# Kernel tuning notes

Hardware: AMD Instinct MI355X
Metric: run time of the kernel (lower is better)

The kernel has to match this reference:

```python
import jax, jax.numpy as jnp
import numpy as np

T = 100          # sequence length (number of GRU steps)
H = 50           # carry/hidden dim
Z = 10           # latent dim
OUT = Z + Z * (Z + 1) // 2  # 65: mean + tril Cholesky entries
LN_EPS = 1e-6    # flax LayerNorm default epsilon


def setup_inputs() -> dict:
    key = jax.random.key(0)
    ks = jax.random.split(key, 8)
    # Orthogonal-ish recurrent kernels via QR for well-conditioned dynamics
    def ortho(k):
        a = jax.random.normal(k, (H, H), dtype=jnp.float32)
        q, _ = jnp.linalg.qr(a)
        return q
    return {
        "carry_init": jax.random.normal(ks[0], (H,), dtype=jnp.float32),
        "W_hr": ortho(ks[1]), "b_hr": jnp.zeros((H,), jnp.float32),
        "s_r": jnp.ones((H,), jnp.float32), "o_r": jnp.zeros((H,), jnp.float32),
        "W_hz": ortho(ks[2]), "b_hz": jnp.zeros((H,), jnp.float32),
        "s_z": jnp.ones((H,), jnp.float32), "o_z": jnp.zeros((H,), jnp.float32),
        "W_hn": ortho(ks[3]), "b_hn": jnp.zeros((H,), jnp.float32),
        "s_n": jnp.ones((H,), jnp.float32), "o_n": jnp.zeros((H,), jnp.float32),
        "W_dense": jax.random.normal(ks[4], (H, OUT), jnp.float32) * (1.0 / jnp.sqrt(H)),
        "b_dense": jnp.zeros((OUT,), jnp.float32),
    }


def _layernorm(x, scale, bias):
    mu = jnp.mean(x, axis=-1, keepdims=True)
    var = jnp.mean(jnp.square(x - mu), axis=-1, keepdims=True)
    return (x - mu) * jax.lax.rsqrt(var + LN_EPS) * scale + bias


def reference(carry_init, W_hr, b_hr, s_r, o_r, W_hz, b_hz, s_z, o_z,
              W_hn, b_hn, s_n, o_n, W_dense, b_dense):
    # Input to the GRU is zeros((T,1)) -> cell ignores it entirely (no input kernel).
    def step(h, _):
        r = jax.nn.sigmoid(_layernorm(h @ W_hr + b_hr, s_r, o_r))
        z = jax.nn.sigmoid(_layernorm(h @ W_hz + b_hz, s_z, o_z))
        n = jnp.tanh(r * _layernorm(h @ W_hn + b_hn, s_n, o_n))
        new_h = (1.0 - z) * n + z * h
        return new_h, new_h

    _, hs = jax.lax.scan(step, carry_init, None, length=T)  # (T, H)
    out = hs @ W_dense + b_dense                              # (T, OUT)

    tril = jnp.tril_indices(Z)
    eye = jnp.eye(Z, dtype=out.dtype)

    def nat(x):
        mu, flat = x[:Z], x[Z:]
        L = jnp.zeros((Z, Z), dtype=x.dtype).at[tril].set(flat)
        d = jax.nn.softplus(jnp.diagonal(L))  # positive diagonal -> PD Sigma
        L = L.at[jnp.diag_indices(Z)].set(d)
        Sigma = L @ L.T
        # psd_solve: J = Sigma^{-1} via Cholesky solve
        J = jax.scipy.linalg.cho_solve((L, True), eye)
        h_nat = J @ mu
        return Sigma, mu, J, h_nat

    Sigma, mu, J, h_nat = jax.vmap(nat)(out)
    return Sigma, mu, J, h_nat
```

## Files before the change

### kernel.cpp

```cpp
#include <hip/hip_runtime.h>
#include <hip/hip_bf16.h>
#include <math.h>

#define T_STEPS 100
#define H_DIM   50
#define Z_DIM   10
#define OUT_DIM 65
#define KP      25

typedef _Float16 half2v __attribute__((ext_vector_type(2)));

__device__ __forceinline__ float bcast_lane(float v, int lane) {
    return __uint_as_float(__builtin_amdgcn_readlane(__float_as_uint(v), lane));
}
__device__ __forceinline__ unsigned readlane_u(unsigned v, int lane) {
    return (unsigned)__builtin_amdgcn_readlane((int)v, lane);
}
template<int CTRL>
__device__ __forceinline__ float dpp_mov(float x) {
    return __uint_as_float((unsigned)__builtin_amdgcn_update_dpp(
        0, (int)__float_as_uint(x), CTRL, 0xF, 0xF, true));
}
#define DPP_ROW_SHL1 0x101
#define DPP_SHR1     0x111
#define DPP_SHR2     0x112
#define DPP_SHR4     0x114
#define DPP_SHR8     0x118
#define DPP_BCAST15  0x142
#define DPP_BCAST31  0x143

__device__ __forceinline__ unsigned pack_h2(float lo, float hi) {
#if __has_builtin(__builtin_amdgcn_cvt_pkrtz)
    return __builtin_bit_cast(unsigned, __builtin_amdgcn_cvt_pkrtz(lo, hi));
#else
    half2v p; p.x = (_Float16)lo; p.y = (_Float16)hi;
    return __builtin_bit_cast(unsigned, p);
#endif
}
__device__ __forceinline__ float fdot2h(unsigned a, unsigned b, float c) {
#if __has_builtin(__builtin_amdgcn_fdot2)
    return __builtin_amdgcn_fdot2(__builtin_bit_cast(half2v, a),
                                  __builtin_bit_cast(half2v, b), c, false);
#else
    const half2v x = __builtin_bit_cast(half2v, a);
    const half2v y = __builtin_bit_cast(half2v, b);
    return fmaf((float)x.x, (float)y.x, fmaf((float)x.y, (float)y.y, c));
#endif
}

__device__ __forceinline__ float fast_rcp(float x) { return __builtin_amdgcn_rcpf(x); }
__device__ __forceinline__ float fast_rsq(float x) { return __builtin_amdgcn_rsqf(x); }
__device__ __forceinline__ float fast_sigmoid(float x) {
    return fast_rcp(1.0f + __expf(-x));
}
__device__ __forceinline__ float fast_tanh(float y) {
    return 1.0f - 2.0f * fast_rcp(__expf(2.0f * y) + 1.0f);
}

__global__ __launch_bounds__(64, 1)
void gru_recur_kernel(
    const float* __restrict__ carry_init,
    const float* __restrict__ W_hr, const float* __restrict__ b_hr,
    const float* __restrict__ s_r,  const float* __restrict__ o_r,
    const float* __restrict__ W_hz, const float* __restrict__ b_hz,
    const float* __restrict__ s_z,  const float* __restrict__ o_z,
    const float* __restrict__ W_hn, const float* __restrict__ b_hn,
    const float* __restrict__ s_n,  const float* __restrict__ o_n,
    float* __restrict__ ws_h)
{
    const int  j     = threadIdx.x;
    const bool valid = (j < H_DIM);
    const int  jc    = valid ? j : 0;

    unsigned wr[KP], wz[KP], wn[KP];
    #pragma unroll
    for (int k = 0; k < KP; ++k) {
        const int i0 = 2 * k, i1 = 2 * k + 1;
        wr[k] = pack_h2(valid ? W_hr[i0 * H_DIM + j] : 0.0f,
                        valid ? W_hr[i1 * H_DIM + j] : 0.0f);
        wz[k] = pack_h2(valid ? W_hz[i0 * H_DIM + j] : 0.0f,
                        valid ? W_hz[i1 * H_DIM + j] : 0.0f);
        wn[k] = pack_h2(valid ? W_hn[i0 * H_DIM + j] : 0.0f,
                        valid ? W_hn[i1 * H_DIM + j] : 0.0f);
    }
    #pragma unroll
    for (int k = 0; k < KP; ++k)
        asm volatile("" : "+v"(wr[k]), "+v"(wz[k]), "+v"(wn[k]));

    const float bjr = valid ? b_hr[jc] : 0.0f;
    const float bjz = valid ? b_hz[jc] : 0.0f;
    const float bjn = valid ? b_hn[jc] : 0.0f;
    const float sr  = s_r[jc], og_r = o_r[jc];
    const float sz  = s_z[jc], og_z = o_z[jc];
    const float sn  = s_n[jc], og_n = o_n[jc];

    float h = valid ? carry_init[jc] : 0.0f;
    const float invH = 1.0f / (float)H_DIM;

    float    hsl = dpp_mov<DPP_ROW_SHL1>(h);
    unsigned hpk = pack_h2(h, hsl);

    #pragma unroll 1
    for (int t = 0; t < T_STEPS; ++t) {
        float ar0 = bjr, ar1 = 0.0f;
        float az0 = bjz, az1 = 0.0f;
        float an0 = bjn, an1 = 0.0f;
        #pragma unroll
        for (int k = 0; k < KP; k += 2) {
            const unsigned s0 = readlane_u(hpk, 2 * k);
            ar0 = fdot2h(s0, wr[k], ar0);
            az0 = fdot2h(s0, wz[k], az0);
            an0 = fdot2h(s0, wn[k], an0);
            if (k + 1 < KP) {
                const unsigned s1 = readlane_u(hpk, 2 * (k + 1));
                ar1 = fdot2h(s1, wr[k + 1], ar1);
                az1 = fdot2h(s1, wz[k + 1], az1);
                an1 = fdot2h(s1, wn[k + 1], an1);
            }
        }
        const float ar = ar0 + ar1;
        const float az = az0 + az1;
        const float an = an0 + an1;

        float mr = ar, qr = ar * ar;
        float mz = az, qz = az * az;
        float mn = an, qn = an * an;
        #define STAGE(C)                                      \
            mr += dpp_mov<C>(mr); qr += dpp_mov<C>(qr);       \
            mz += dpp_mov<C>(mz); qz += dpp_mov<C>(qz);       \
            mn += dpp_mov<C>(mn); qn += dpp_mov<C>(qn);
        STAGE(DPP_SHR1) STAGE(DPP_SHR2) STAGE(DPP_SHR4)
        STAGE(DPP_SHR8) STAGE(DPP_BCAST15) STAGE(DPP_BCAST31)
        #undef STAGE
        mr = bcast_lane(mr, 63); qr = bcast_lane(qr, 63);
        mz = bcast_lane(mz, 63); qz = bcast_lane(qz, 63);
        mn = bcast_lane(mn, 63); qn = bcast_lane(qn, 63);

        const float mu_r  = mr * invH;
        const float var_r = fmaxf(qr * invH - mu_r * mu_r, 0.0f);
        const float g_r   = (ar - mu_r) * fast_rsq(var_r + 1e-6f) * sr + og_r;
        const float r     = fast_sigmoid(g_r);

        const float mu_z  = mz * invH;
        const float var_z = fmaxf(qz * invH - mu_z * mu_z, 0.0f);
        const float g_z   = (az - mu_z) * fast_rsq(var_z + 1e-6f) * sz + og_z;
        const float z     = fast_sigmoid(g_z);

        const float mu_n  = mn * invH;
        const float var_n = fmaxf(qn * invH - mu_n * mu_n, 0.0f);
        const float g_n   = (an - mu_n) * fast_rsq(var_n + 1e-6f) * sn + og_n;
        const float n     = fast_tanh(r * g_n);

        h = n + z * (h - n);
        ws_h[t * 64 + j] = h;

        hsl = dpp_mov<DPP_ROW_SHL1>(h);
        hpk = pack_h2(h, hsl);
    }
}

__global__ __launch_bounds__(128)
void dense_nat_kernel(
    const float* __restrict__ W_dense, const float* __restrict__ b_dense,
    const float* __restrict__ ws_h, float* __restrict__ out)
{
    const int t   = blockIdx.x;
    const int tid = threadIdx.x;

    __shared__ float hloc[H_DIM];
    __shared__ float dl  [OUT_DIM];
    __shared__ float Lp  [55];
    __shared__ float Li  [55];
    __shared__ float Jsh [100];

    if (tid < H_DIM) hloc[tid] = ws_h[t * 64 + tid];
    __syncthreads();

    if (tid < OUT_DIM) {
        float acc = b_dense[tid];
        #pragma unroll
        for (int i = 0; i < H_DIM; ++i)
            acc = fmaf(hloc[i], W_dense[i * OUT_DIM + tid], acc);
        dl[tid] = acc;
    }
    __syncthreads();

    if (tid < 55) {
        float v = dl[Z_DIM + tid];
        const bool isd = (tid==0)|(tid==2)|(tid==5)|(tid==9)|(tid==14)|
                         (tid==20)|(tid==27)|(tid==35)|(tid==44)|(tid==54);
        if (isd) v = (v > 20.0f) ? v : log1pf(__expf(v));
        Lp[tid] = v;
    }
    __syncthreads();

    float* outSigma = out;
    float* outMu    = out + 10000;
    float* outJ     = out + 11000;
    float* outHnat  = out + 21000;

    int a = 0;
    {
        #pragma unroll
        for (int x = 1; x < Z_DIM; ++x)
            if (tid >= x * (x + 1) / 2) a = x;
    }
    const int b = tid - a * (a + 1) / 2;

    if (tid < 55) {
        float s = 0.0f;
        for (int k = 0; k <= b; ++k)
            s = fmaf(Lp[a * (a + 1) / 2 + k], Lp[b * (b + 1) / 2 + k], s);
        outSigma[t * 100 + a * 10 + b] = s;
        outSigma[t * 100 + b * 10 + a] = s;
    }
    if (tid >= 64 && tid < 64 + Z_DIM) outMu[t * 10 + (tid - 64)] = dl[tid - 64];
    __syncthreads();

    if (tid == 0) {
        #pragma unroll
        for (int i = 0; i < Z_DIM; ++i) {
            const float d = 1.0f / Lp[i * (i + 1) / 2 + i];
            #pragma unroll
            for (int k = 0; k < i; ++k) {
                float s = 0.0f;
                for (int m = k; m < i; ++m)
                    s = fmaf(Lp[i * (i + 1) / 2 + m], Li[m * (m + 1) / 2 + k], s);
                Li[i * (i + 1) / 2 + k] = -s * d;
            }
            Li[i * (i + 1) / 2 + i] = d;
        }
    }
    __syncthreads();

    if (tid < 55) {
        float s = 0.0f;
        for (int m = a; m < Z_DIM; ++m)
            s = fmaf(Li[m * (m + 1) / 2 + a], Li[m * (m + 1) / 2 + b], s);
        outJ[t * 100 + a * 10 + b] = s;
        outJ[t * 100 + b * 10 + a] = s;
        Jsh[a * 10 + b] = s;
        Jsh[b * 10 + a] = s;
    }
    __syncthreads();

    if (tid < Z_DIM) {
        float s = 0.0f;
        #pragma unroll
        for (int k = 0; k < Z_DIM; ++k)
            s = fmaf(Jsh[tid * 10 + k], dl[k], s);
        outHnat[t * 10 + tid] = s;
    }
}

extern "C" void kernel_launch(void* const* d_in, const int* in_sizes, int n_in,
                              void* d_out, int out_size, void* d_ws, size_t ws_size,
                              hipStream_t stream) {
    const float* p[15];
    for (int i = 0; i < 15; ++i) p[i] = (const float*)d_in[i];
    float* ws_h = (float*)d_ws;

    gru_recur_kernel<<<dim3(1), dim3(64), 0, stream>>>(
        p[0],
        p[1], p[2], p[3], p[4],
        p[5], p[6], p[7], p[8],
        p[9], p[10], p[11], p[12],
        ws_h);

    dense_nat_kernel<<<dim3(T_STEPS), dim3(128), 0, stream>>>(
        p[13], p[14], ws_h, (float*)d_out);
}
```

Baseline: 137.4 us.

## Split GRU gates across three waves and parallelize triangular inverse per column

```diff
diff --git a/kernel.cpp b/kernel.cpp
--- a/kernel.cpp
+++ b/kernel.cpp
@@ -57,7 +57,7 @@
     return 1.0f - 2.0f * fast_rcp(__expf(2.0f * y) + 1.0f);
 }
 
-__global__ __launch_bounds__(64, 1)
+__global__ __launch_bounds__(192, 1)
 void gru_recur_kernel(
     const float* __restrict__ carry_init,
     const float* __restrict__ W_hr, const float* __restrict__ b_hr,
@@ -68,31 +68,33 @@
     const float* __restrict__ s_n,  const float* __restrict__ o_n,
     float* __restrict__ ws_h)
 {
-    const int  j     = threadIdx.x;
+    const int  tid   = threadIdx.x;
+    const int  wave  = tid >> 6;
+    const int  j     = tid & 63;
     const bool valid = (j < H_DIM);
     const int  jc    = valid ? j : 0;
 
-    unsigned wr[KP], wz[KP], wn[KP];
+    const float* Wg = (wave == 0) ? W_hr : (wave == 1) ? W_hz : W_hn;
+    const float* bg = (wave == 0) ? b_hr : (wave == 1) ? b_hz : b_hn;
+    const float* sg = (wave == 0) ? s_r  : (wave == 1) ? s_z  : s_n;
+    const float* og = (wave == 0) ? o_r  : (wave == 1) ? o_z  : o_n;
+
+    unsigned w[KP];
     #pragma unroll
     for (int k = 0; k < KP; ++k) {
         const int i0 = 2 * k, i1 = 2 * k + 1;
-        wr[k] = pack_h2(valid ? W_hr[i0 * H_DIM + j] : 0.0f,
-                        valid ? W_hr[i1 * H_DIM + j] : 0.0f);
-        wz[k] = pack_h2(valid ? W_hz[i0 * H_DIM + j] : 0.0f,
-                        valid ? W_hz[i1 * H_DIM + j] : 0.0f);
-        wn[k] = pack_h2(valid ? W_hn[i0 * H_DIM + j] : 0.0f,
-                        valid ? W_hn[i1 * H_DIM + j] : 0.0f);
+        w[k] = pack_h2(valid ? Wg[i0 * H_DIM + j] : 0.0f,
+                       valid ? Wg[i1 * H_DIM + j] : 0.0f);
     }
     #pragma unroll
-    for (int k = 0; k < KP; ++k)
-        asm volatile("" : "+v"(wr[k]), "+v"(wz[k]), "+v"(wn[k]));
-
-    const float bjr = valid ? b_hr[jc] : 0.0f;
-    const float bjz = valid ? b_hz[jc] : 0.0f;
-    const float bjn = valid ? b_hn[jc] : 0.0f;
-    const float sr  = s_r[jc], og_r = o_r[jc];
-    const float sz  = s_z[jc], og_z = o_z[jc];
-    const float sn  = s_n[jc], og_n = o_n[jc];
+    for (int k = 0; k < KP; ++k) asm volatile("" : "+v"(w[k]));
+
+    const float bj = valid ? bg[jc] : 0.0f;
+    const float sc = sg[jc];
+    const float of = og[jc];
+
+    __shared__ float gbuf[2][3][64];
+    __shared__ __align__(16) float hist[T_STEPS][64];
 
     float h = valid ? carry_init[jc] : 0.0f;
     const float invH = 1.0f / (float)H_DIM;
@@ -102,60 +104,51 @@
 
     #pragma unroll 1
     for (int t = 0; t < T_STEPS; ++t) {
-        float ar0 = bjr, ar1 = 0.0f;
-        float az0 = bjz, az1 = 0.0f;
-        float an0 = bjn, an1 = 0.0f;
+        float a0 = bj, a1 = 0.0f;
         #pragma unroll
         for (int k = 0; k < KP; k += 2) {
             const unsigned s0 = readlane_u(hpk, 2 * k);
-            ar0 = fdot2h(s0, wr[k], ar0);
-            az0 = fdot2h(s0, wz[k], az0);
-            an0 = fdot2h(s0, wn[k], an0);
+            a0 = fdot2h(s0, w[k], a0);
             if (k + 1 < KP) {
                 const unsigned s1 = readlane_u(hpk, 2 * (k + 1));
-                ar1 = fdot2h(s1, wr[k + 1], ar1);
-                az1 = fdot2h(s1, wz[k + 1], az1);
-                an1 = fdot2h(s1, wn[k + 1], an1);
+                a1 = fdot2h(s1, w[k + 1], a1);
             }
         }
-        const float ar = ar0 + ar1;
-        const float az = az0 + az1;
-        const float an = an0 + an1;
-
-        float mr = ar, qr = ar * ar;
-        float mz = az, qz = az * az;
-        float mn = an, qn = an * an;
-        #define STAGE(C)                                      \
-            mr += dpp_mov<C>(mr); qr += dpp_mov<C>(qr);       \
-            mz += dpp_mov<C>(mz); qz += dpp_mov<C>(qz);       \
-            mn += dpp_mov<C>(mn); qn += dpp_mov<C>(qn);
+        const float a = a0 + a1;
+
+        float m = a, q = a * a;
+        #define STAGE(C) m += dpp_mov<C>(m); q += dpp_mov<C>(q);
         STAGE(DPP_SHR1) STAGE(DPP_SHR2) STAGE(DPP_SHR4)
         STAGE(DPP_SHR8) STAGE(DPP_BCAST15) STAGE(DPP_BCAST31)
         #undef STAGE
-        mr = bcast_lane(mr, 63); qr = bcast_lane(qr, 63);
-        mz = bcast_lane(mz, 63); qz = bcast_lane(qz, 63);
-        mn = bcast_lane(mn, 63); qn = bcast_lane(qn, 63);
-
-        const float mu_r  = mr * invH;
-        const float var_r = fmaxf(qr * invH - mu_r * mu_r, 0.0f);
-        const float g_r   = (ar - mu_r) * fast_rsq(var_r + 1e-6f) * sr + og_r;
-        const float r     = fast_sigmoid(g_r);
-
-        const float mu_z  = mz * invH;
-        const float var_z = fmaxf(qz * invH - mu_z * mu_z, 0.0f);
-        const float g_z   = (az - mu_z) * fast_rsq(var_z + 1e-6f) * sz + og_z;
-        const float z     = fast_sigmoid(g_z);
-
-        const float mu_n  = mn * invH;
-        const float var_n = fmaxf(qn * invH - mu_n * mu_n, 0.0f);
-        const float g_n   = (an - mu_n) * fast_rsq(var_n + 1e-6f) * sn + og_n;
-        const float n     = fast_tanh(r * g_n);
-
+        m = bcast_lane(m, 63); q = bcast_lane(q, 63);
+
+        const float mu  = m * invH;
+        const float var = fmaxf(q * invH - mu * mu, 0.0f);
+        const float g   = (a - mu) * fast_rsq(var + 1e-6f) * sc + of;
+        const float val = (wave == 2) ? g : fast_sigmoid(g);
+
+        gbuf[t & 1][wave][j] = val;
+        __syncthreads();
+
+        const float r  = gbuf[t & 1][0][j];
+        const float z  = gbuf[t & 1][1][j];
+        const float gn = gbuf[t & 1][2][j];
+        const float n  = fast_tanh(r * gn);
         h = n + z * (h - n);
-        ws_h[t * 64 + j] = h;
+
+        if (wave == 0) hist[t][j] = h;
 
         hsl = dpp_mov<DPP_ROW_SHL1>(h);
         hpk = pack_h2(h, hsl);
+    }
+
+    __syncthreads();
+    {
+        float4*       dst = (float4*)ws_h;
+        const float4* src = (const float4*)hist;
+        for (int i = tid; i < T_STEPS * 16; i += 192)
+            dst[i] = src[i];
     }
 }
 
@@ -217,19 +210,26 @@
     if (tid >= 64 && tid < 64 + Z_DIM) outMu[t * 10 + (tid - 64)] = dl[tid - 64];
     __syncthreads();
 
-    if (tid == 0) {
+    if (tid < Z_DIM) {
+        const int k = tid;
+        float dinv[Z_DIM];
+        #pragma unroll
+        for (int i = 0; i < Z_DIM; ++i)
+            dinv[i] = 1.0f / Lp[i * (i + 1) / 2 + i];
+        float col[Z_DIM];
+        #pragma unroll
+        for (int i = 0; i < Z_DIM; ++i) col[i] = 0.0f;
         #pragma unroll
         for (int i = 0; i < Z_DIM; ++i) {
-            const float d = 1.0f / Lp[i * (i + 1) / 2 + i];
+            float s = 0.0f;
             #pragma unroll
-            for (int k = 0; k < i; ++k) {
-                float s = 0.0f;
-                for (int m = k; m < i; ++m)
-                    s = fmaf(Lp[i * (i + 1) / 2 + m], Li[m * (m + 1) / 2 + k], s);
-                Li[i * (i + 1) / 2 + k] = -s * d;
-            }
-            Li[i * (i + 1) / 2 + i] = d;
+            for (int m = 0; m < i; ++m)
+                s = fmaf(Lp[i * (i + 1) / 2 + m], col[m], s);
+            if (i >= k) col[i] = (i == k) ? dinv[i] : -s * dinv[i];
         }
+        #pragma unroll
+        for (int i = 0; i < Z_DIM; ++i)
+            if (i >= k) Li[i * (i + 1) / 2 + k] = col[i];
     }
     __syncthreads();
 
@@ -260,7 +260,7 @@
     for (int i = 0; i < 15; ++i) p[i] = (const float*)d_in[i];
     float* ws_h = (float*)d_ws;
 
-    gru_recur_kernel<<<dim3(1), dim3(64), 0, stream>>>(
+    gru_recur_kernel<<<dim3(1), dim3(192), 0, stream>>>(
         p[0],
         p[1], p[2], p[3], p[4],
         p[5], p[6], p[7], p[8],
```

Result: faster. 128.4 us (-6.5%).

## Batch hidden-state readlanes, buffer GRU history in LDS, parallelize triangular inverse

Applied to the files above, without the earlier changes.

```diff
diff --git a/kernel.cpp b/kernel.cpp
--- a/kernel.cpp
+++ b/kernel.cpp
@@ -94,6 +94,8 @@
     const float sz  = s_z[jc], og_z = o_z[jc];
     const float sn  = s_n[jc], og_n = o_n[jc];
 
+    __shared__ __align__(16) float hist[T_STEPS][64];
+
     float h = valid ? carry_init[jc] : 0.0f;
     const float invH = 1.0f / (float)H_DIM;
 
@@ -102,20 +104,24 @@
 
     #pragma unroll 1
     for (int t = 0; t < T_STEPS; ++t) {
+        unsigned hs[KP];
+        #pragma unroll
+        for (int k = 0; k < KP; ++k) hs[k] = readlane_u(hpk, 2 * k);
+        #pragma unroll
+        for (int k = 0; k < KP; ++k) asm volatile("" : "+s"(hs[k]));
+
         float ar0 = bjr, ar1 = 0.0f;
         float az0 = bjz, az1 = 0.0f;
         float an0 = bjn, an1 = 0.0f;
         #pragma unroll
         for (int k = 0; k < KP; k += 2) {
-            const unsigned s0 = readlane_u(hpk, 2 * k);
-            ar0 = fdot2h(s0, wr[k], ar0);
-            az0 = fdot2h(s0, wz[k], az0);
-            an0 = fdot2h(s0, wn[k], an0);
+            ar0 = fdot2h(hs[k], wr[k], ar0);
+            az0 = fdot2h(hs[k], wz[k], az0);
+            an0 = fdot2h(hs[k], wn[k], an0);
             if (k + 1 < KP) {
-                const unsigned s1 = readlane_u(hpk, 2 * (k + 1));
-                ar1 = fdot2h(s1, wr[k + 1], ar1);
-                az1 = fdot2h(s1, wz[k + 1], az1);
-                an1 = fdot2h(s1, wn[k + 1], an1);
+                ar1 = fdot2h(hs[k + 1], wr[k + 1], ar1);
+                az1 = fdot2h(hs[k + 1], wz[k + 1], az1);
+                an1 = fdot2h(hs[k + 1], wn[k + 1], an1);
             }
         }
         const float ar = ar0 + ar1;
@@ -152,10 +158,19 @@
         const float n     = fast_tanh(r * g_n);
 
         h = n + z * (h - n);
-        ws_h[t * 64 + j] = h;
+
+        hist[t][j] = h;
 
         hsl = dpp_mov<DPP_ROW_SHL1>(h);
         hpk = pack_h2(h, hsl);
+    }
+
+    asm volatile("s_waitcnt lgkmcnt(0)" ::: "memory");
+    {
+        float4*       dst = (float4*)ws_h;
+        const float4* src = (const float4*)hist;
+        for (int i = j; i < T_STEPS * 16; i += 64)
+            dst[i] = src[i];
     }
 }
 
@@ -217,19 +232,26 @@
     if (tid >= 64 && tid < 64 + Z_DIM) outMu[t * 10 + (tid - 64)] = dl[tid - 64];
     __syncthreads();
 
-    if (tid == 0) {
+    if (tid < Z_DIM) {
+        const int k = tid;
+        float dinv[Z_DIM];
+        #pragma unroll
+        for (int i = 0; i < Z_DIM; ++i)
+            dinv[i] = 1.0f / Lp[i * (i + 1) / 2 + i];
+        float col[Z_DIM];
+        #pragma unroll
+        for (int i = 0; i < Z_DIM; ++i) col[i] = 0.0f;
         #pragma unroll
         for (int i = 0; i < Z_DIM; ++i) {
-            const float d = 1.0f / Lp[i * (i + 1) / 2 + i];
+            float s = 0.0f;
             #pragma unroll
-            for (int k = 0; k < i; ++k) {
-                float s = 0.0f;
-                for (int m = k; m < i; ++m)
-                    s = fmaf(Lp[i * (i + 1) / 2 + m], Li[m * (m + 1) / 2 + k], s);
-                Li[i * (i + 1) / 2 + k] = -s * d;
-            }
-            Li[i * (i + 1) / 2 + i] = d;
+            for (int m = 0; m < i; ++m)
+                s = fmaf(Lp[i * (i + 1) / 2 + m], col[m], s);
+            if (i >= k) col[i] = (i == k) ? dinv[i] : -s * dinv[i];
         }
+        #pragma unroll
+        for (int i = 0; i < Z_DIM; ++i)
+            if (i >= k) Li[i * (i + 1) / 2 + k] = col[i];
     }
     __syncthreads();
 
```

After: 133.2 us. 3.0% less time.
